# Performance work log

Hardware: AMD Instinct MI355X
Metric: run time of the kernel (lower is better)

The kernel has to match this reference:

```python
import jax, jax.numpy as jnp
import numpy as np

B = 4
POINT_NUM = 50000
N_VOXELS = 150000
FEAT_DIM = 256


def setup_inputs() -> dict:
    key = jax.random.key(0)
    k1, k2, k3, k4 = jax.random.split(key, 4)
    backbone_features = jax.random.normal(k1, (N_VOXELS, FEAT_DIM), dtype=jnp.float32)
    quantize2original = jax.random.randint(k2, (B * POINT_NUM,), 0, N_VOXELS, dtype=jnp.int64)
    # Conv1d(FEAT_DIM, 2, kernel_size=1) weight [2, FEAT_DIM] and bias [2]
    fan_in = FEAT_DIM
    bound = 1.0 / np.sqrt(fan_in)
    w_scoring = jax.random.uniform(k3, (2, FEAT_DIM), minval=-bound, maxval=bound, dtype=jnp.float32)
    b_scoring = jax.random.uniform(k4, (2,), minval=-bound, maxval=bound, dtype=jnp.float32)
    return {
        'backbone_features': backbone_features,
        'quantize2original': quantize2original,
        'w_scoring': w_scoring,
        'b_scoring': b_scoring,
    }


def reference(backbone_features, quantize2original, w_scoring, b_scoring):
    # Gather realign: voxel features -> original point order  [B*P, C]
    seed_features = backbone_features[quantize2original]
    # [B, P, C] -> [B, C, P]
    seed_features = seed_features.reshape(B, POINT_NUM, FEAT_DIM).transpose(0, 2, 1)
    # 1x1 Conv1d scoring head: [B, 2, P]
    suction_score = jnp.einsum('oc,bcp->bop', w_scoring, seed_features) + b_scoring[None, :, None]
    seal_score_pred = suction_score[:, 0]    # [B, P]
    wrench_score_pred = suction_score[:, 1]  # [B, P]
    return seal_score_pred, wrench_score_pred
```

## Files before the change

kernel.cpp:

```cpp
#include <hip/hip_runtime.h>

#define BATCH 4
#define POINT_NUM 50000
#define NPTS (BATCH * POINT_NUM)
#define NVOX 150000
#define FEAT 256

__global__ __launch_bounds__(256) void fused_score_kernel(
    const float* __restrict__ feat,
    const int*   __restrict__ idx,
    const float* __restrict__ w,
    const float* __restrict__ bias,
    float* __restrict__ out)
{
    const int wave = (blockIdx.x * blockDim.x + threadIdx.x) >> 6;
    const int lane = threadIdx.x & 63;
    if (wave >= NPTS) return;

    const int v = idx[wave];

    const float4 w0 = ((const float4*)(w))[lane];
    const float4 w1 = ((const float4*)(w + FEAT))[lane];

    const float4 f = ((const float4*)(feat + (size_t)v * FEAT))[lane];

    float a = f.x * w0.x + f.y * w0.y + f.z * w0.z + f.w * w0.w;
    float b = f.x * w1.x + f.y * w1.y + f.z * w1.z + f.w * w1.w;

    #pragma unroll
    for (int off = 32; off > 0; off >>= 1) {
        a += __shfl_down(a, off, 64);
        b += __shfl_down(b, off, 64);
    }

    if (lane == 0) {
        out[wave]        = a + bias[0];
        out[NPTS + wave] = b + bias[1];
    }
}

extern "C" void kernel_launch(void* const* d_in, const int* in_sizes, int n_in,
                              void* d_out, int out_size, void* d_ws, size_t ws_size,
                              hipStream_t stream) {
    const float* feat = (const float*)d_in[0];
    const int*   idx  = (const int*)d_in[1];
    const float* w    = (const float*)d_in[2];
    const float* bias = (const float*)d_in[3];
    float* out = (float*)d_out;

    (void)d_ws; (void)ws_size;

    const int blocks = (NPTS * 64 + 255) / 256;
    fused_score_kernel<<<blocks, 256, 0, stream>>>(feat, idx, w, bias, out);
}
```

Before: 238.3 us.

## Score each voxel once, then gather scores via cooperative grid sync

Rather than gathering a full 256-float feature row for each of the 200k points, the kernel first computes the two scores for all 150k voxels with a sequential, coalesced sweep that handles two rows per wave iteration. After a grid-wide sync it gathers the per-voxel scores by index into the output. This removes redundant dot products and random row gathers, in exchange for a cooperative launch, a grid barrier and a workspace round trip. It also scores every voxel, including ones no point references.

Result: slower. 332.7 us (+39.6%).

```diff
diff --git a/kernel.cpp b/kernel.cpp
--- a/kernel.cpp
+++ b/kernel.cpp
@@ -1,4 +1,7 @@
 #include <hip/hip_runtime.h>
+#include <hip/hip_cooperative_groups.h>
+
+namespace cg = cooperative_groups;
 
 #define BATCH 4
 #define POINT_NUM 50000
@@ -6,36 +9,70 @@
 #define NVOX 150000
 #define FEAT 256
 
-__global__ __launch_bounds__(256) void fused_score_kernel(
+#define NBLOCKS 1024
+#define TPB 256
+#define NWAVES (NBLOCKS * (TPB / 64))
+
+__global__ __launch_bounds__(TPB, 4) void fused_coop(
     const float* __restrict__ feat,
     const int*   __restrict__ idx,
     const float* __restrict__ w,
     const float* __restrict__ bias,
+    float* __restrict__ s0,
+    float* __restrict__ s1,
     float* __restrict__ out)
 {
-    const int wave = (blockIdx.x * blockDim.x + threadIdx.x) >> 6;
+    cg::grid_group grid = cg::this_grid();
+
+    const int tid  = blockIdx.x * TPB + threadIdx.x;
+    const int wave = tid >> 6;
     const int lane = threadIdx.x & 63;
-    if (wave >= NPTS) return;
-
-    const int v = idx[wave];
 
     const float4 w0 = ((const float4*)(w))[lane];
     const float4 w1 = ((const float4*)(w + FEAT))[lane];
+    const float b0 = bias[0];
+    const float b1 = bias[1];
 
-    const float4 f = ((const float4*)(feat + (size_t)v * FEAT))[lane];
+    for (int row = wave; row < NVOX; row += 2 * NWAVES) {
+        const int row2 = row + NWAVES;
+        const bool has2 = (row2 < NVOX);
 
-    float a = f.x * w0.x + f.y * w0.y + f.z * w0.z + f.w * w0.w;
-    float b = f.x * w1.x + f.y * w1.y + f.z * w1.z + f.w * w1.w;
+        const float4 f1 = ((const float4*)(feat + (size_t)row * FEAT))[lane];
+        float4 f2;
+        if (has2) f2 = ((const float4*)(feat + (size_t)row2 * FEAT))[lane];
 
-    #pragma unroll
-    for (int off = 32; off > 0; off >>= 1) {
-        a += __shfl_down(a, off, 64);
-        b += __shfl_down(b, off, 64);
+        float a1 = f1.x * w0.x + f1.y * w0.y + f1.z * w0.z + f1.w * w0.w;
+        float c1 = f1.x * w1.x + f1.y * w1.y + f1.z * w1.z + f1.w * w1.w;
+        float a2 = 0.f, c2 = 0.f;
+        if (has2) {
+            a2 = f2.x * w0.x + f2.y * w0.y + f2.z * w0.z + f2.w * w0.w;
+            c2 = f2.x * w1.x + f2.y * w1.y + f2.z * w1.z + f2.w * w1.w;
+        }
+
+        #pragma unroll
+        for (int off = 32; off > 0; off >>= 1) {
+            a1 += __shfl_down(a1, off, 64);
+            c1 += __shfl_down(c1, off, 64);
+            a2 += __shfl_down(a2, off, 64);
+            c2 += __shfl_down(c2, off, 64);
+        }
+
+        if (lane == 0) {
+            s0[row] = a1 + b0;
+            s1[row] = c1 + b1;
+            if (has2) {
+                s0[row2] = a2 + b0;
+                s1[row2] = c2 + b1;
+            }
+        }
     }
 
-    if (lane == 0) {
-        out[wave]        = a + bias[0];
-        out[NPTS + wave] = b + bias[1];
+    grid.sync();
+
+    for (int p = tid; p < NPTS; p += NBLOCKS * TPB) {
+        const int v = idx[p];
+        out[p]        = s0[v];
+        out[NPTS + p] = s1[v];
     }
 }
 
@@ -48,8 +85,11 @@
     const float* bias = (const float*)d_in[3];
     float* out = (float*)d_out;
 
-    (void)d_ws; (void)ws_size;
+    float* s0 = (float*)d_ws;
+    float* s1 = s0 + NVOX;
 
-    const int blocks = (NPTS * 64 + 255) / 256;
-    fused_score_kernel<<<blocks, 256, 0, stream>>>(feat, idx, w, bias, out);
+    void* args[] = { (void*)&feat, (void*)&idx, (void*)&w, (void*)&bias,
+                     (void*)&s0, (void*)&s1, (void*)&out };
+    hipLaunchCooperativeKernel((void*)fused_coop, dim3(NBLOCKS), dim3(TPB),
+                               args, 0, stream);
 }
```
